# Performance work log

Hardware: AMD Instinct MI355X
Metric: run time of the kernel (lower is better)

Reference implementation:

```python
import jax, jax.numpy as jnp
import numpy as np

THETA = 10000.0


def _rope_tables(T, head_dim, dtype):
    # w = 1/theta^(arange(1, d+1, 2)[:d//2] / d); positions start at 1 (matches source)
    exps = jnp.arange(1, head_dim + 1, 2, dtype=jnp.float32)[: head_dim // 2] / head_dim
    w = 1.0 / (THETA ** exps)
    t = jnp.arange(1, T + 1, dtype=jnp.float32)
    angles = t[:, None] * w[None, :]  # [T, d/2]
    return jnp.sin(angles).astype(dtype), jnp.cos(angles).astype(dtype)


def _rotate(x, sin, cos):
    # x: [..., T, d], sin/cos: [T, d/2]; rotate interleaved len-2 subvectors
    x1 = x[..., ::2]
    x2 = x[..., 1::2]
    x1p = x1 * cos - x2 * sin
    x2p = x1 * sin + x2 * cos
    return jnp.stack((x1p, x2p), axis=-1).reshape(x.shape)


def setup_inputs() -> dict:
    key = jax.random.key(0)
    B, Tq, Tkv, C = 4, 2048, 2048, 1024
    k1, k2, k3, k4, k5 = jax.random.split(key, 5)
    s = 1.0 / np.sqrt(C)
    return {
        "x_q": jax.random.normal(k1, (B, Tq, C), dtype=jnp.float32),
        "x_kv": jax.random.normal(k2, (B, Tkv, C), dtype=jnp.float32),
        "q_tok_mask": jnp.ones((B, Tq), dtype=bool),
        "kv_tok_mask": jnp.ones((B, Tkv), dtype=bool),
        "W_q": jax.random.normal(k3, (C, C), dtype=jnp.float32) * s,
        "W_kv": jax.random.normal(k4, (C, 2 * C), dtype=jnp.float32) * s,
        "W_c": jax.random.normal(k5, (C, C), dtype=jnp.float32) * s,
    }


def reference(x_q, x_kv, q_tok_mask, kv_tok_mask, W_q, W_kv, W_c):
    B, Tq, C = x_q.shape
    Tkv = x_kv.shape[1]
    H = 16
    D = C // H  # head_dim = 64

    q = (x_q @ W_q).reshape(B, Tq, H, D).transpose(0, 2, 1, 3)      # [B,H,Tq,D]
    kv = x_kv @ W_kv                                                  # [B,Tkv,2C]
    k, v = kv[..., :C], kv[..., C:]
    k = k.reshape(B, Tkv, H, D).transpose(0, 2, 1, 3)                 # [B,H,Tkv,D]
    v = v.reshape(B, Tkv, H, D).transpose(0, 2, 1, 3)

    sin_q, cos_q = _rope_tables(Tq, D, x_q.dtype)
    sin_k, cos_k = _rope_tables(Tkv, D, x_q.dtype)
    q = _rotate(q, sin_q, cos_q)
    k = _rotate(k, sin_k, cos_k)

    att = jnp.einsum("bhqd,bhkd->bhqk", q, k) / jnp.sqrt(jnp.asarray(D, x_q.dtype))
    mask = (q_tok_mask[:, :, None] & kv_tok_mask[:, None, :])[:, None, :, :]  # [B,1,Tq,Tkv]
    att = jnp.where(mask, att, jnp.asarray(-1e9, att.dtype))
    att = jax.nn.softmax(att, axis=-1)

    y = jnp.einsum("bhqk,bhkd->bhqd", att, v)                         # [B,H,Tq,D]
    y = y.transpose(0, 2, 1, 3).reshape(B, Tq, C)
    return y @ W_c
```

## Files before the change

kernel.cpp:

```cpp
#include <hip/hip_runtime.h>
#include <hip/hip_bf16.h>
#include <math.h>

typedef float f32x4 __attribute__((ext_vector_type(4)));
typedef short bf16x8 __attribute__((ext_vector_type(8)));

#define DEVINL __device__ __forceinline__

DEVINL unsigned short f2bf(float f) {
  unsigned int u = __float_as_uint(f);
  return (unsigned short)((u + 0x7FFFu + ((u >> 16) & 1u)) >> 16);
}
DEVINL float bf2f(unsigned short h) { return __uint_as_float(((unsigned int)h) << 16); }

DEVINL unsigned int pack_bf2(float f0, float f1) {
  unsigned int u0 = __float_as_uint(f0) + 0x8000u;
  unsigned int u1 = __float_as_uint(f1) + 0x8000u;
#if __has_builtin(__builtin_amdgcn_perm)
  return __builtin_amdgcn_perm(u1, u0, 0x07060302u);
#else
  return (u0 >> 16) | (u1 & 0xffff0000u);
#endif
}

DEVINL unsigned int cvtpk_bf2(float f0, float f1) {
  unsigned int r;
  asm("v_cvt_pk_bf16_f32 %0, %1, %2" : "=v"(r) : "v"(f0), "v"(f1));
  return r;
}

DEVINL float fast_exp2(float x) {
#if __has_builtin(__builtin_amdgcn_exp2f)
  return __builtin_amdgcn_exp2f(x);
#else
  return exp2f(x);
#endif
}

DEVINL void glds16(const unsigned short* g, unsigned short* l) {
  __builtin_amdgcn_global_load_lds(
      (const __attribute__((address_space(1))) void*)g,
      (__attribute__((address_space(3))) void*)l, 16, 0, 0);
}

__global__ void cvt2(const float* __restrict__ a, const float* __restrict__ b,
                     unsigned short* __restrict__ da, unsigned short* __restrict__ db,
                     int n8half) {
  int halfgrid = gridDim.x >> 1;
  int hi = blockIdx.x >= halfgrid;
  const float* src = hi ? b : a;
  unsigned short* dst = hi ? db : da;
  int bx = blockIdx.x - (hi ? halfgrid : 0);
  int stride = halfgrid * blockDim.x;
  for (int i = bx * blockDim.x + threadIdx.x; i < n8half; i += stride) {
    float4 x = ((const float4*)src)[2*i];
    float4 y = ((const float4*)src)[2*i + 1];
    union { unsigned short us[8]; uint4 v; } u;
    u.us[0]=f2bf(x.x); u.us[1]=f2bf(x.y); u.us[2]=f2bf(x.z); u.us[3]=f2bf(x.w);
    u.us[4]=f2bf(y.x); u.us[5]=f2bf(y.y); u.us[6]=f2bf(y.z); u.us[7]=f2bf(y.w);
    ((uint4*)dst)[i] = u.v;
  }
}

__global__ void transpose3(const float* __restrict__ Wq, const float* __restrict__ Wkv,
                           const float* __restrict__ Wc,
                           unsigned short* __restrict__ dq, unsigned short* __restrict__ dkv,
                           unsigned short* __restrict__ dc) {
  __shared__ float tile[32][33];
  int bx = blockIdx.x;
  const float* src; unsigned short* dst; int N;
  if (bx < 32)      { src = Wq;  dst = dq;  N = 1024; }
  else if (bx < 96) { src = Wkv; dst = dkv; N = 2048; bx -= 32; }
  else              { src = Wc;  dst = dc;  N = 1024; bx -= 96; }
  const int K = 1024;
  int n0 = bx * 32, k0 = blockIdx.y * 32;
  int tx = threadIdx.x, ty = threadIdx.y;
  for (int i = 0; i < 4; ++i) {
    int k = ty + i * 8;
    tile[k][tx] = src[(long)(k0 + k) * N + n0 + tx];
  }
  __syncthreads();
  for (int i = 0; i < 4; ++i) {
    int n = ty + i * 8;
    dst[(long)(n0 + n) * K + k0 + tx] = f2bf(tile[tx][n]);
  }
}

struct GemmCtx {
  int lane, lo16, quad, wm, wn;
  int r0, soff, ldsoff, fc;
};
DEVINL void gemm_core(const unsigned short* __restrict__ A, const unsigned short* __restrict__ Bt,
                      int m0, int n0, int K,
                      unsigned short* As, unsigned short* Bs,
                      const GemmCtx& c, f32x4 acc[4][4]) {
  int aoff[4], boff[4];
  for (int mt = 0; mt < 4; ++mt) aoff[mt] = (c.wm * 64 + mt * 16 + c.lo16) * 32 + c.fc;
  for (int nt = 0; nt < 4; ++nt) boff[nt] = (c.wn * 64 + nt * 16 + c.lo16) * 32 + c.fc;
  for (int k0 = 0; k0 < K; k0 += 32) {
    glds16(A  + (long)(m0 + c.r0)      * K + k0 + c.soff, As + c.ldsoff);
    glds16(A  + (long)(m0 + 64 + c.r0) * K + k0 + c.soff, As + 2048 + c.ldsoff);
    glds16(Bt + (long)(n0 + c.r0)      * K + k0 + c.soff, Bs + c.ldsoff);
    glds16(Bt + (long)(n0 + 64 + c.r0) * K + k0 + c.soff, Bs + 2048 + c.ldsoff);
    __syncthreads();
    bf16x8 af[4], bfv[4];
    for (int mt = 0; mt < 4; ++mt) af[mt]  = *(const bf16x8*)(As + aoff[mt]);
    for (int nt = 0; nt < 4; ++nt) bfv[nt] = *(const bf16x8*)(Bs + boff[nt]);
    for (int mt = 0; mt < 4; ++mt)
      for (int nt = 0; nt < 4; ++nt)
        acc[mt][nt] = __builtin_amdgcn_mfma_f32_16x16x32_bf16(af[mt], bfv[nt], acc[mt][nt], 0, 0, 0);
    __syncthreads();
  }
}
DEVINL GemmCtx make_ctx(int tid) {
  GemmCtx c;
  int wave = tid >> 6; c.lane = tid & 63;
  c.lo16 = c.lane & 15; c.quad = c.lane >> 4;
  c.wm = wave >> 1; c.wn = wave & 1;
  c.r0 = wave * 16 + (c.lane >> 2);
  c.soff = ((c.lane & 3) ^ ((c.lane >> 3) & 3)) * 8;
  c.ldsoff = wave * 512 + c.lane * 8;
  c.fc = (c.quad ^ ((c.lo16 >> 1) & 3)) * 8;
  return c;
}

__global__ __launch_bounds__(256) void gemm_qkv(
    const unsigned short* __restrict__ xq, const unsigned short* __restrict__ xkv,
    const unsigned short* __restrict__ wq, const unsigned short* __restrict__ wkv,
    unsigned short* __restrict__ qout, unsigned short* __restrict__ kout,
    unsigned short* __restrict__ vout, float qscale) {
  __shared__ unsigned short As[128 * 32];
  __shared__ unsigned short Bs[128 * 32];
  const bool isq = blockIdx.x < 8;
  const unsigned short* A  = isq ? xq : xkv;
  const unsigned short* Bt = isq ? wq : wkv;
  const int n0 = (isq ? blockIdx.x : (blockIdx.x - 8)) * 128;
  const int m0 = blockIdx.y * 128;
  GemmCtx c = make_ctx(threadIdx.x);
  f32x4 acc[4][4];
  f32x4 zero = {0.f, 0.f, 0.f, 0.f};
  for (int i = 0; i < 4; ++i) for (int j = 0; j < 4; ++j) acc[i][j] = zero;
  gemm_core(A, Bt, m0, n0, 1024, As, Bs, c, acc);

  const bool isv = (!isq) && (n0 >= 1024);
  const float LOG2_10000_64 = 0.20762050593046f;

  if (!isv) {
    unsigned short* out = isq ? qout : kout;
    const float scale = isq ? qscale : 1.0f;
    const float sgn = (c.lo16 & 1) ? 1.0f : -1.0f;
    for (int nt = 0; nt < 4; ++nt) {
      int gn = n0 + c.wn * 64 + nt * 16 + c.lo16;
      int d = gn & 63, h = gn >> 6;
      float w = fast_exp2(-(float)(2 * (d >> 1) + 1) * LOG2_10000_64);
      for (int mt = 0; mt < 4; ++mt) {
        int gmb = m0 + c.wm * 64 + mt * 16 + c.quad * 4;
        for (int r = 0; r < 4; ++r) {
          int gm = gmb + r;
          int b = gm >> 11, t = gm & 2047;
          float v = acc[mt][nt][r];
          float p = __shfl_xor(v, 1, 64);
          float sa, ca; __sincosf((float)(t + 1) * w, &sa, &ca);
          float res = fmaf(p, sgn * sa, v * ca) * scale;
          out[((long)((b * 16 + h) * 2048 + t)) * 64 + d] = f2bf(res);
        }
      }
    }
  } else {
    for (int mt = 0; mt < 4; ++mt) {
      int gmb = m0 + c.wm * 64 + mt * 16 + c.quad * 4;
      for (int nt = 0; nt < 4; ++nt) {
        int gn = n0 + c.wn * 64 + nt * 16 + c.lo16 - 1024;
        int h = gn >> 6, d = gn & 63;
        for (int r = 0; r < 4; ++r) {
          int gm = gmb + r;
          int b = gm >> 11, t = gm & 2047;
          int u = t & 31;
          int tp = (t & ~31) | (8 * ((u >> 2) & 3) + (u & 3) + 4 * (u >> 4));
          vout[((long)((b * 16 + h) * 64 + d)) * 2048 + tp] = f2bf(acc[mt][nt][r]);
        }
      }
    }
  }
}

__global__ __launch_bounds__(256) void gemm_out(
    const unsigned short* __restrict__ A, const unsigned short* __restrict__ Bt,
    float* __restrict__ out) {
  __shared__ unsigned short As[128 * 32];
  __shared__ unsigned short Bs[128 * 32];
  const int m0 = blockIdx.y * 128, n0 = blockIdx.x * 128;
  GemmCtx c = make_ctx(threadIdx.x);
  f32x4 acc[4][4];
  f32x4 zero = {0.f, 0.f, 0.f, 0.f};
  for (int i = 0; i < 4; ++i) for (int j = 0; j < 4; ++j) acc[i][j] = zero;
  gemm_core(A, Bt, m0, n0, 1024, As, Bs, c, acc);
  for (int mt = 0; mt < 4; ++mt) {
    int gmb = m0 + c.wm * 64 + mt * 16 + c.quad * 4;
    for (int nt = 0; nt < 4; ++nt) {
      int gn = n0 + c.wn * 64 + nt * 16 + c.lo16;
      for (int r = 0; r < 4; ++r)
        out[(long)(gmb + r) * 1024 + gn] = acc[mt][nt][r];
    }
  }
}

__global__ __launch_bounds__(128, 4) void flash_st(
    const unsigned short* __restrict__ Q, const unsigned short* __restrict__ Kr,
    const unsigned short* __restrict__ Vt, unsigned short* __restrict__ Y) {
  __shared__ unsigned short Ks[64 * 64];
  __shared__ unsigned short Vs[64 * 64];
  const int tid  = threadIdx.x;
  const int wave = tid >> 6, lane = tid & 63;
  const int lo16 = lane & 15, quad = lane >> 4;

  const int lin = blockIdx.x;
  const int xcd = lin & 7, pos = lin >> 3;
  const int bh  = xcd * 8 + (pos >> 5);
  const int yt  = pos & 31;
  const int b = bh >> 4, h = bh & 15;
  const int q0 = yt * 64 + wave * 32;

  bf16x8 qf[2][2];
  for (int qt = 0; qt < 2; ++qt)
    for (int dk = 0; dk < 2; ++dk)
      qf[qt][dk] = *(const bf16x8*)(Q + ((long)bh * 2048 + q0 + qt * 16 + lo16) * 64 + dk * 32 + quad * 8);

  f32x4 zero = {0.f, 0.f, 0.f, 0.f};
  f32x4 o[4][2];
  f32x4 lacc[2];
  for (int dt = 0; dt < 4; ++dt) for (int qt = 0; qt < 2; ++qt) o[dt][qt] = zero;
  for (int qt = 0; qt < 2; ++qt) lacc[qt] = zero;

  const int sr = lane >> 3;
  const int gc = ((lane & 7) ^ sr) * 8;

  for (int kb = 0; kb < 2048; kb += 64) {
    for (int p = 0; p < 4; ++p) {
      int g = p * 2 + wave;
      int r = g * 8 + sr;
      glds16(Kr + ((long)bh * 2048 + kb + r) * 64 + gc, Ks + g * 512 + lane * 8);
      glds16(Vt + ((long)bh * 64 + r) * 2048 + kb + gc, Vs + g * 512 + lane * 8);
    }
    __syncthreads();

    for (int ks = 0; ks < 2; ++ks) {
      unsigned int pu[2][4];
      for (int ktl = 0; ktl < 2; ++ktl) {
        const int krow = (ks * 2 + ktl) * 16 + lo16;
        const int x7 = krow & 7;
        bf16x8 ka0 = *(const bf16x8*)(Ks + krow * 64 + ((quad ^ x7) * 8));
        bf16x8 ka1 = *(const bf16x8*)(Ks + krow * 64 + (((4 + quad) ^ x7) * 8));
        for (int qt = 0; qt < 2; ++qt) {
          f32x4 s = zero;
          __builtin_amdgcn_s_setprio(1);
          s = __builtin_amdgcn_mfma_f32_16x16x32_bf16(ka0, qf[qt][0], s, 0, 0, 0);
          s = __builtin_amdgcn_mfma_f32_16x16x32_bf16(ka1, qf[qt][1], s, 0, 0, 0);
          __builtin_amdgcn_s_setprio(0);
          f32x4 e;
          e[0] = fast_exp2(s[0]); e[1] = fast_exp2(s[1]);
          e[2] = fast_exp2(s[2]); e[3] = fast_exp2(s[3]);
          lacc[qt] += e;
          pu[qt][ktl * 2 + 0] = cvtpk_bf2(e[0], e[1]);
          pu[qt][ktl * 2 + 1] = cvtpk_bf2(e[2], e[3]);
        }
      }
      bf16x8 pbv[2];
      for (int qt = 0; qt < 2; ++qt) {
        union { unsigned int u[4]; bf16x8 v; } pb;
        pb.u[0] = pu[qt][0]; pb.u[1] = pu[qt][1];
        pb.u[2] = pu[qt][2]; pb.u[3] = pu[qt][3];
        pbv[qt] = pb.v;
      }
      for (int dt = 0; dt < 4; ++dt) {
        const int vrow = dt * 16 + lo16;
        bf16x8 va = *(const bf16x8*)(Vs + vrow * 64 + (((ks * 4 + quad) ^ (vrow & 7)) * 8));
        __builtin_amdgcn_s_setprio(1);
        for (int qt = 0; qt < 2; ++qt)
          o[dt][qt] = __builtin_amdgcn_mfma_f32_16x16x32_bf16(va, pbv[qt], o[dt][qt], 0, 0, 0);
        __builtin_amdgcn_s_setprio(0);
      }
    }
    __syncthreads();
  }

  float rl[2];
  for (int qt = 0; qt < 2; ++qt) {
    float l = (lacc[qt][0] + lacc[qt][1]) + (lacc[qt][2] + lacc[qt][3]);
    l += __shfl_xor(l, 16, 64);
    l += __shfl_xor(l, 32, 64);
    rl[qt] = 1.0f / l;
  }

  for (int dt = 0; dt < 4; ++dt)
    for (int qt = 0; qt < 2; ++qt) {
      float v0 = o[dt][qt][0] * rl[qt], v1 = o[dt][qt][1] * rl[qt];
      float v2 = o[dt][qt][2] * rl[qt], v3 = o[dt][qt][3] * rl[qt];
      uint2 pk; pk.x = cvtpk_bf2(v0, v1); pk.y = cvtpk_bf2(v2, v3);
      long row = (long)b * 2048 + q0 + qt * 16 + lo16;
      int col = h * 64 + dt * 16 + quad * 4;
      *(uint2*)(Y + row * 1024 + col) = pk;
    }
}

extern "C" void kernel_launch(void* const* d_in, const int* in_sizes, int n_in,
                              void* d_out, int out_size, void* d_ws, size_t ws_size,
                              hipStream_t stream) {
  const float* x_q  = (const float*)d_in[0];
  const float* x_kv = (const float*)d_in[1];
  const float* W_q  = (const float*)d_in[4];
  const float* W_kv = (const float*)d_in[5];
  const float* W_c  = (const float*)d_in[6];

  char* ws = (char*)d_ws;
  const size_t MB = 1u << 20;
  unsigned short* xq_bf  = (unsigned short*)(ws + 0);
  unsigned short* xkv_bf = (unsigned short*)(ws + 16 * MB);
  unsigned short* wq_t   = (unsigned short*)(ws + 32 * MB);
  unsigned short* wkv_t  = (unsigned short*)(ws + 34 * MB);
  unsigned short* wc_t   = (unsigned short*)(ws + 38 * MB);
  unsigned short* q_r    = (unsigned short*)(ws + 40 * MB);
  unsigned short* k_r    = (unsigned short*)(ws + 56 * MB);
  unsigned short* v_t    = (unsigned short*)(ws + 72 * MB);
  unsigned short* y      = xq_bf;

  const float QSCALE = 0.125f * 1.44269504088896f;

  dim3 tb(32, 8);
  cvt2<<<2048, 256, 0, stream>>>(x_q, x_kv, xq_bf, xkv_bf, 1048576);
  transpose3<<<dim3(128, 32), tb, 0, stream>>>(W_q, W_kv, W_c, wq_t, wkv_t, wc_t);
  gemm_qkv<<<dim3(24, 64), 256, 0, stream>>>(xq_bf, xkv_bf, wq_t, wkv_t, q_r, k_r, v_t, QSCALE);
  flash_st<<<dim3(2048), 128, 0, stream>>>(q_r, k_r, v_t, y);
  gemm_out<<<dim3(8, 64), 256, 0, stream>>>(y, wc_t, (float*)d_out);
}
```

Measured before the change: 319.5 us.

## Replace QKV projection GEMM with 256x256-tile double-buffered 512-thread kernel

The fused QKV projection GEMM moves from 128x128 tiles with 256 threads to 256x256 tiles with 512 threads. Each K step is 64 wide, loaded asynchronously from global memory into double-buffered LDS with an XOR swizzle, and the MFMA loop raises wave priority. The goal is more operand reuse per tile and overlap of loads with compute. The cost is 128 KB of LDS per block, so only one block fits per CU, and with 384 blocks the grid has a partial second wave. The RoPE and V-transpose epilogues keep their logic and are re-indexed for the larger tile.

```diff
diff --git a/kernel.cpp b/kernel.cpp
--- a/kernel.cpp
+++ b/kernel.cpp
@@ -12,16 +12,6 @@
   return (unsigned short)((u + 0x7FFFu + ((u >> 16) & 1u)) >> 16);
 }
 DEVINL float bf2f(unsigned short h) { return __uint_as_float(((unsigned int)h) << 16); }
-
-DEVINL unsigned int pack_bf2(float f0, float f1) {
-  unsigned int u0 = __float_as_uint(f0) + 0x8000u;
-  unsigned int u1 = __float_as_uint(f1) + 0x8000u;
-#if __has_builtin(__builtin_amdgcn_perm)
-  return __builtin_amdgcn_perm(u1, u0, 0x07060302u);
-#else
-  return (u0 >> 16) | (u1 & 0xffff0000u);
-#endif
-}
 
 DEVINL unsigned int cvtpk_bf2(float f0, float f1) {
   unsigned int r;
@@ -124,41 +114,94 @@
   return c;
 }
 
-__global__ __launch_bounds__(256) void gemm_qkv(
+__global__ __launch_bounds__(512, 2) void gemm_qkv256(
     const unsigned short* __restrict__ xq, const unsigned short* __restrict__ xkv,
     const unsigned short* __restrict__ wq, const unsigned short* __restrict__ wkv,
     unsigned short* __restrict__ qout, unsigned short* __restrict__ kout,
     unsigned short* __restrict__ vout, float qscale) {
-  __shared__ unsigned short As[128 * 32];
-  __shared__ unsigned short Bs[128 * 32];
-  const bool isq = blockIdx.x < 8;
+  __shared__ unsigned short lds[2][2][256 * 64];
+  const int tid  = threadIdx.x;
+  const int wave = tid >> 6, lane = tid & 63;
+  const int lo16 = lane & 15, quad = lane >> 4;
+  const int wm = wave >> 2, wn = wave & 3;
+
+  const int x = blockIdx.x;
+  const bool isq = x < 4;
   const unsigned short* A  = isq ? xq : xkv;
   const unsigned short* Bt = isq ? wq : wkv;
-  const int n0 = (isq ? blockIdx.x : (blockIdx.x - 8)) * 128;
-  const int m0 = blockIdx.y * 128;
-  GemmCtx c = make_ctx(threadIdx.x);
-  f32x4 acc[4][4];
+  const long brow0 = isq ? (long)x * 256 : (long)(x - 4) * 256;
+  const long m0 = (long)blockIdx.y * 256;
+
+  const int sr = lane >> 3;
+  const int ch = ((lane & 7) ^ sr) * 8;
+
+#define STAGE256(K0, BUF) do {                                              \
+    unsigned short* Al = &lds[BUF][0][0];                                   \
+    unsigned short* Bl = &lds[BUF][1][0];                                   \
+    for (int p = 0; p < 4; ++p) {                                           \
+      long r = p * 64 + wave * 8 + sr;                                      \
+      int dst = (p * 8 + wave) * 512 + lane * 8;                            \
+      glds16(A  + (m0 + r) * 1024 + (K0) + ch, Al + dst);                   \
+      glds16(Bt + (brow0 + r) * 1024 + (K0) + ch, Bl + dst);                \
+    } } while (0)
+
+  f32x4 acc[8][4];
   f32x4 zero = {0.f, 0.f, 0.f, 0.f};
-  for (int i = 0; i < 4; ++i) for (int j = 0; j < 4; ++j) acc[i][j] = zero;
-  gemm_core(A, Bt, m0, n0, 1024, As, Bs, c, acc);
-
-  const bool isv = (!isq) && (n0 >= 1024);
+  for (int i = 0; i < 8; ++i) for (int j = 0; j < 4; ++j) acc[i][j] = zero;
+
+  STAGE256(0, 0);
+
+  for (int t = 0; t < 16; ++t) {
+    if (t + 1 < 16) {
+      STAGE256((t + 1) * 64, (t + 1) & 1);
+      asm volatile("s_waitcnt vmcnt(8)" ::: "memory");
+    } else {
+      asm volatile("s_waitcnt vmcnt(0)" ::: "memory");
+    }
+    __builtin_amdgcn_s_barrier();
+    asm volatile("" ::: "memory");
+    const unsigned short* Ab = &lds[t & 1][0][0];
+    const unsigned short* Bb = &lds[t & 1][1][0];
+
+    for (int kc = 0; kc < 2; ++kc) {
+      bf16x8 bfr[4], afr[8];
+      for (int nf = 0; nf < 4; ++nf) {
+        int r = wn * 64 + nf * 16 + lo16;
+        bfr[nf] = *(const bf16x8*)(Bb + r * 64 + (((kc * 4 + quad) ^ (r & 7)) * 8));
+      }
+      for (int mf = 0; mf < 8; ++mf) {
+        int r = wm * 128 + mf * 16 + lo16;
+        afr[mf] = *(const bf16x8*)(Ab + r * 64 + (((kc * 4 + quad) ^ (r & 7)) * 8));
+      }
+      __builtin_amdgcn_s_setprio(1);
+      for (int mf = 0; mf < 8; ++mf)
+        for (int nf = 0; nf < 4; ++nf)
+          acc[mf][nf] = __builtin_amdgcn_mfma_f32_16x16x32_bf16(afr[mf], bfr[nf], acc[mf][nf], 0, 0, 0);
+      __builtin_amdgcn_s_setprio(0);
+    }
+    asm volatile("" ::: "memory");
+    __builtin_amdgcn_s_barrier();
+  }
+#undef STAGE256
+
+  const bool isv = (!isq) && (brow0 >= 1024);
+  const long col0 = isq ? (long)x * 256 : (isv ? brow0 - 1024 : brow0);
   const float LOG2_10000_64 = 0.20762050593046f;
 
   if (!isv) {
     unsigned short* out = isq ? qout : kout;
     const float scale = isq ? qscale : 1.0f;
-    const float sgn = (c.lo16 & 1) ? 1.0f : -1.0f;
-    for (int nt = 0; nt < 4; ++nt) {
-      int gn = n0 + c.wn * 64 + nt * 16 + c.lo16;
+    const float sgn = (lo16 & 1) ? 1.0f : -1.0f;
+    for (int nf = 0; nf < 4; ++nf) {
+      int gn = (int)col0 + wn * 64 + nf * 16 + lo16;
       int d = gn & 63, h = gn >> 6;
       float w = fast_exp2(-(float)(2 * (d >> 1) + 1) * LOG2_10000_64);
-      for (int mt = 0; mt < 4; ++mt) {
-        int gmb = m0 + c.wm * 64 + mt * 16 + c.quad * 4;
+      for (int mf = 0; mf < 8; ++mf) {
+        int gmb = (int)m0 + wm * 128 + mf * 16 + quad * 4;
         for (int r = 0; r < 4; ++r) {
           int gm = gmb + r;
           int b = gm >> 11, t = gm & 2047;
-          float v = acc[mt][nt][r];
+          float v = acc[mf][nf][r];
           float p = __shfl_xor(v, 1, 64);
           float sa, ca; __sincosf((float)(t + 1) * w, &sa, &ca);
           float res = fmaf(p, sgn * sa, v * ca) * scale;
@@ -167,17 +210,17 @@
       }
     }
   } else {
-    for (int mt = 0; mt < 4; ++mt) {
-      int gmb = m0 + c.wm * 64 + mt * 16 + c.quad * 4;
-      for (int nt = 0; nt < 4; ++nt) {
-        int gn = n0 + c.wn * 64 + nt * 16 + c.lo16 - 1024;
+    for (int mf = 0; mf < 8; ++mf) {
+      int gmb = (int)m0 + wm * 128 + mf * 16 + quad * 4;
+      for (int nf = 0; nf < 4; ++nf) {
+        int gn = (int)col0 + wn * 64 + nf * 16 + lo16;
         int h = gn >> 6, d = gn & 63;
         for (int r = 0; r < 4; ++r) {
           int gm = gmb + r;
           int b = gm >> 11, t = gm & 2047;
           int u = t & 31;
           int tp = (t & ~31) | (8 * ((u >> 2) & 3) + (u & 3) + 4 * (u >> 4));
-          vout[((long)((b * 16 + h) * 64 + d)) * 2048 + tp] = f2bf(acc[mt][nt][r]);
+          vout[((long)((b * 16 + h) * 64 + d)) * 2048 + tp] = f2bf(acc[mf][nf][r]);
         }
       }
     }
@@ -329,7 +372,7 @@
   dim3 tb(32, 8);
   cvt2<<<2048, 256, 0, stream>>>(x_q, x_kv, xq_bf, xkv_bf, 1048576);
   transpose3<<<dim3(128, 32), tb, 0, stream>>>(W_q, W_kv, W_c, wq_t, wkv_t, wc_t);
-  gemm_qkv<<<dim3(24, 64), 256, 0, stream>>>(xq_bf, xkv_bf, wq_t, wkv_t, q_r, k_r, v_t, QSCALE);
+  gemm_qkv256<<<dim3(12, 32), 512, 0, stream>>>(xq_bf, xkv_bf, wq_t, wkv_t, q_r, k_r, v_t, QSCALE);
   flash_st<<<dim3(2048), 128, 0, stream>>>(q_r, k_r, v_t, y);
   gemm_out<<<dim3(8, 64), 256, 0, stream>>>(y, wc_t, (float*)d_out);
 }
```

Result: slower. 414.3 us (+29.6%).
